# Kernel optimization log

Measured on AMD Instinct MI355X. Metric: run time of the kernel, lower is better.

Reference implementation:

```python
import jax, jax.numpy as jnp
import numpy as np

N_NODES = 50000
N_EDGES = 800000
N_GRAPHS = 64
EPS = 1e-5
NEG_SLOPE = 0.2


def gat_conv(x, src, dst, W, a_src, a_dst, bias, heads, ch):
    # x: [N, Fin]; W: [Fin, heads*ch]; a_src/a_dst: [heads, ch]; bias: [heads*ch]
    N = x.shape[0]
    h = (x @ W).reshape(N, heads, ch)                       # [N,H,C]
    s_src = jnp.sum(h * a_src, axis=-1)                     # [N,H]
    s_dst = jnp.sum(h * a_dst, axis=-1)                     # [N,H]
    scores = jax.nn.leaky_relu(s_src[src] + s_dst[dst], NEG_SLOPE)  # [E,H]
    m = jax.ops.segment_max(scores, dst, num_segments=N)    # segment softmax (stable)
    e = jnp.exp(scores - m[dst])
    denom = jax.ops.segment_sum(e, dst, num_segments=N)
    alpha = e / denom[dst]                                  # [E,H]
    msg = h[src] * alpha[:, :, None]                        # [E,H,C]
    out = jax.ops.segment_sum(msg, dst, num_segments=N)     # [N,H,C]
    return out.reshape(N, heads * ch) + bias


def batch_norm(x, gamma, beta):
    mu = jnp.mean(x, axis=0)
    var = jnp.var(x, axis=0)  # biased, as in torch BN forward (training mode)
    return gamma * (x - mu) * jax.lax.rsqrt(var + EPS) + beta


def setup_inputs() -> dict:
    key = jax.random.key(0)
    ks = jax.random.split(key, 20)
    x = jax.random.normal(ks[0], (N_NODES, 8), dtype=jnp.float32)
    edge_index = jax.random.randint(ks[1], (2, N_EDGES), 0, N_NODES, dtype=jnp.int32)
    batch = jnp.sort(jax.random.randint(ks[2], (N_NODES,), 0, N_GRAPHS, dtype=jnp.int32))
    g = lambda k, shape: jax.random.normal(k, shape, dtype=jnp.float32) * 0.1
    return {
        "x": x, "edge_index": edge_index, "batch": batch,
        "W1": g(ks[3], (8, 128)), "a_src1": g(ks[4], (4, 32)), "a_dst1": g(ks[5], (4, 32)),
        "b1": jnp.zeros((128,), jnp.float32), "g1": jnp.ones((128,), jnp.float32),
        "beta1": jnp.zeros((128,), jnp.float32),
        "W2": g(ks[6], (128, 256)), "a_src2": g(ks[7], (4, 64)), "a_dst2": g(ks[8], (4, 64)),
        "b2": jnp.zeros((256,), jnp.float32), "g2": jnp.ones((256,), jnp.float32),
        "beta2": jnp.zeros((256,), jnp.float32),
        "fc1_w": g(ks[9], (256, 128)), "fc1_b": jnp.zeros((128,), jnp.float32),
        "fc2_w": g(ks[10], (128, 64)), "fc2_b": jnp.zeros((64,), jnp.float32),
        "fc3_w": g(ks[11], (64, 1)), "fc3_b": jnp.zeros((1,), jnp.float32),
    }


def reference(x, edge_index, batch, W1, a_src1, a_dst1, b1, g1, beta1,
              W2, a_src2, a_dst2, b2, g2, beta2,
              fc1_w, fc1_b, fc2_w, fc2_b, fc3_w, fc3_b):
    N = x.shape[0]
    loop = jnp.arange(N, dtype=edge_index.dtype)
    src = jnp.concatenate([edge_index[0], loop])  # PyG GATConv adds self-loops
    dst = jnp.concatenate([edge_index[1], loop])

    h = gat_conv(x, src, dst, W1, a_src1, a_dst1, b1, heads=4, ch=32)
    h = jax.nn.elu(batch_norm(h, g1, beta1))
    h = gat_conv(h, src, dst, W2, a_src2, a_dst2, b2, heads=4, ch=64)
    h = jax.nn.elu(batch_norm(h, g2, beta2))

    # global mean pool over graphs
    sums = jax.ops.segment_sum(h, batch, num_segments=N_GRAPHS)
    counts = jax.ops.segment_sum(jnp.ones((N,), h.dtype), batch, num_segments=N_GRAPHS)
    pooled = sums / jnp.maximum(counts, 1.0)[:, None]       # [G,256]

    z = jax.nn.relu(pooled @ fc1_w + fc1_b)
    emb = jax.nn.relu(z @ fc2_w + fc2_b)
    out = emb @ fc3_w + fc3_b
    return out.reshape(-1)
```

## Files before the change

kernel.cpp:

```cpp
#include <hip/hip_runtime.h>
#include <hip/hip_bf16.h>
#include <cmath>

#define NSLOPE 0.2f
#define BN_EPS 1e-5f
#define DEGCAP 128

static __device__ __forceinline__ float lrelu(float v) { return v > 0.f ? v : NSLOPE * v; }

static __device__ __forceinline__ float wmax64(float v) {
#pragma unroll
  for (int off = 32; off; off >>= 1) v = fmaxf(v, __shfl_xor(v, off));
  return v;
}
static __device__ __forceinline__ float wsum64(float v) {
#pragma unroll
  for (int off = 32; off; off >>= 1) v += __shfl_xor(v, off);
  return v;
}
static __device__ __forceinline__ unsigned short f2bf(float x) {
  __hip_bfloat16 h = __float2bfloat16(x);
  union { __hip_bfloat16 h; unsigned short u; } c; c.h = h; return c.u;
}
static __device__ __forceinline__ unsigned pack_bf16(float x, float y) {
  return (unsigned)f2bf(x) | ((unsigned)f2bf(y) << 16);
}
static __device__ __forceinline__ float bflo(unsigned p) { return __uint_as_float(p << 16); }
static __device__ __forceinline__ float bfhi(unsigned p) { return __uint_as_float(p & 0xffff0000u); }

__global__ void k_scatter(const int* __restrict__ esrc, const int* __restrict__ edst,
                          const int* __restrict__ batch, int E, int N,
                          int* __restrict__ cnt, int* __restrict__ srcs,
                          int* __restrict__ gstart,
                          const float* __restrict__ W1, const float* __restrict__ as1,
                          const float* __restrict__ ad1, const float* __restrict__ W2,
                          const float* __restrict__ as2, const float* __restrict__ ad2,
                          float* __restrict__ q1s, float* __restrict__ q1d,
                          float* __restrict__ q2s, float* __restrict__ q2d) {
  if (blockIdx.x == 0) {
    int t = threadIdx.x;
    if (t < 32) {
      int k = t >> 2, h = t & 3;
      float s = 0.f, d = 0.f;
      for (int c = 0; c < 32; ++c) {
        float w = W1[k * 128 + h * 32 + c];
        s = fmaf(w, as1[h * 32 + c], s);
        d = fmaf(w, ad1[h * 32 + c], d);
      }
      q1s[t] = s; q1d[t] = d;
    }
    for (int idx = t; idx < 512; idx += 256) {
      int k = idx >> 2, h = idx & 3;
      float s = 0.f, d = 0.f;
      for (int c = 0; c < 64; ++c) {
        float w = W2[k * 256 + h * 64 + c];
        s = fmaf(w, as2[h * 64 + c], s);
        d = fmaf(w, ad2[h * 64 + c], d);
      }
      q2s[idx] = s; q2d[idx] = d;
    }
  }
  int i = blockIdx.x * blockDim.x + threadIdx.x;
  int stride = gridDim.x * blockDim.x;
  int total = E + N;
  for (int j = i; j < total; j += stride) {
    int s, d;
    if (j < E) {
      s = esrc[j]; d = edst[j];
    } else {
      int n = j - E;
      s = n; d = n;
      int b = batch[n];
      if (n == 0) {
        for (int g = 0; g <= b; ++g) gstart[g] = 0;
      } else {
        int pb = batch[n - 1];
        if (pb != b)
          for (int g = pb + 1; g <= b; ++g) gstart[g] = n;
      }
      if (n == N - 1)
        for (int g = b + 1; g <= 64; ++g) gstart[g] = N;
    }
    int pos = atomicAdd(&cnt[d], 1);
    if (pos < DEGCAP) srcs[(size_t)d * DEGCAP + pos] = s;
  }
}

__global__ __launch_bounds__(256) void k_s1(const float* __restrict__ x,
                                            const float* __restrict__ q1s,
                                            const float* __restrict__ q1d,
                                            float* __restrict__ ssrc, float* __restrict__ sdst,
                                            int N) {
  __shared__ float qs[32], qd[32];
  int t = threadIdx.x;
  if (t < 32) { qs[t] = q1s[t]; qd[t] = q1d[t]; }
  __syncthreads();
  for (int n = blockIdx.x * 256 + t; n < N; n += gridDim.x * 256) {
    float4 x0 = *(const float4*)&x[n * 8];
    float4 x1 = *(const float4*)&x[n * 8 + 4];
    float xs[8] = {x0.x, x0.y, x0.z, x0.w, x1.x, x1.y, x1.z, x1.w};
    float4 rs = make_float4(0.f, 0.f, 0.f, 0.f);
    float4 rd = make_float4(0.f, 0.f, 0.f, 0.f);
#pragma unroll
    for (int k = 0; k < 8; ++k) {
      rs.x = fmaf(xs[k], qs[k * 4 + 0], rs.x);
      rs.y = fmaf(xs[k], qs[k * 4 + 1], rs.y);
      rs.z = fmaf(xs[k], qs[k * 4 + 2], rs.z);
      rs.w = fmaf(xs[k], qs[k * 4 + 3], rs.w);
      rd.x = fmaf(xs[k], qd[k * 4 + 0], rd.x);
      rd.y = fmaf(xs[k], qd[k * 4 + 1], rd.y);
      rd.z = fmaf(xs[k], qd[k * 4 + 2], rd.z);
      rd.w = fmaf(xs[k], qd[k * 4 + 3], rd.w);
    }
    *(float4*)&ssrc[n * 4] = rs;
    *(float4*)&sdst[n * 4] = rd;
  }
}

__global__ __launch_bounds__(256) void k_agg1(const float* __restrict__ x,
                                              const float* __restrict__ ssrc,
                                              const float* __restrict__ sdst,
                                              const int* __restrict__ cnt,
                                              const int* __restrict__ srcs,
                                              float* __restrict__ agg , int N) {
  int tid = blockIdx.x * 256 + threadIdx.x;
  int n = tid >> 2, h = tid & 3;
  if (n >= N) return;
  int beg = n * DEGCAP;
  int end = beg + min(cnt[n], DEGCAP);
  float sd = sdst[n * 4 + h];
  float m = -INFINITY;
  for (int e = beg; e < end; ++e) {
    int s = srcs[e];
    m = fmaxf(m, lrelu(ssrc[s * 4 + h] + sd));
  }
  float d = 0.f;
  float acc[8];
#pragma unroll
  for (int k = 0; k < 8; ++k) acc[k] = 0.f;
  const float4* x4 = (const float4*)x;
  for (int e = beg; e < end; ++e) {
    int s = srcs[e];
    float w = expf(lrelu(ssrc[s * 4 + h] + sd) - m);
    d += w;
    float4 xa = x4[(size_t)s * 2];
    float4 xb = x4[(size_t)s * 2 + 1];
    acc[0] = fmaf(w, xa.x, acc[0]); acc[1] = fmaf(w, xa.y, acc[1]);
    acc[2] = fmaf(w, xa.z, acc[2]); acc[3] = fmaf(w, xa.w, acc[3]);
    acc[4] = fmaf(w, xb.x, acc[4]); acc[5] = fmaf(w, xb.y, acc[5]);
    acc[6] = fmaf(w, xb.z, acc[6]); acc[7] = fmaf(w, xb.w, acc[7]);
  }
  float inv = 1.0f / d;
  float4 oA = make_float4(acc[0] * inv, acc[1] * inv, acc[2] * inv, acc[3] * inv);
  float4 oB = make_float4(acc[4] * inv, acc[5] * inv, acc[6] * inv, acc[7] * inv);
  *(float4*)&agg[n * 32 + h * 8] = oA;
  *(float4*)&agg[n * 32 + h * 8 + 4] = oB;
}

__global__ __launch_bounds__(128) void k_stats1(const float* __restrict__ agg,
                                                const float* __restrict__ W1,
                                                const float* __restrict__ b1,
                                                float* __restrict__ part, int N) {
  int t = threadIdx.x;
  __shared__ float ag[32];
  float bb = b1[t];
  float wc[8];
#pragma unroll
  for (int k = 0; k < 8; ++k) wc[k] = W1[k * 128 + t];
  int h = t >> 5;
  float s = 0.f, s2 = 0.f;
  for (int n = blockIdx.x; n < N; n += gridDim.x) {
    if (t < 32) ag[t] = agg[n * 32 + t];
    __syncthreads();
    float v = bb;
#pragma unroll
    for (int k = 0; k < 8; ++k) v = fmaf(ag[h * 8 + k], wc[k], v);
    s += v; s2 += v * v;
    __syncthreads();
  }
  part[(size_t)blockIdx.x * 256 + t] = s;
  part[(size_t)blockIdx.x * 256 + 128 + t] = s2;
}

template <int NB, int TWO_F>
__global__ __launch_bounds__(256) void k_bnreduce2(const float* __restrict__ part,
                                                   float* __restrict__ stat) {
  int j = blockIdx.x, t = threadIdx.x;
  float s = 0.f;
  for (int b = t; b < NB; b += 256) s += part[(size_t)b * TWO_F + j];
#pragma unroll
  for (int off = 32; off; off >>= 1) s += __shfl_xor(s, off);
  __shared__ float red[4];
  if ((t & 63) == 0) red[t >> 6] = s;
  __syncthreads();
  if (t == 0) stat[j] = (red[0] + red[1]) + (red[2] + red[3]);
}

__global__ __launch_bounds__(256) void k_bns2(const float* __restrict__ agg,
                                              const float* __restrict__ W1,
                                              const float* __restrict__ b1,
                                              unsigned* __restrict__ a1h_u,
                                              const float* __restrict__ sum,
                                              const float* __restrict__ sq,
                                              const float* __restrict__ gamma,
                                              const float* __restrict__ beta,
                                              const float* __restrict__ q2s,
                                              const float* __restrict__ q2d,
                                              float* __restrict__ ssrc2,
                                              float* __restrict__ sdst2, int N) {
  int w = threadIdx.x >> 6, l = threadIdx.x & 63;
  int n = blockIdx.x * 4 + w;
  if (n >= N) return;
  int c0 = 2 * l, c1 = 2 * l + 1;
  int h = l >> 4;
  float ag[8];
#pragma unroll
  for (int k = 0; k < 8; ++k) ag[k] = agg[n * 32 + h * 8 + k];
  float v0 = b1[c0], v1 = b1[c1];
#pragma unroll
  for (int k = 0; k < 8; ++k) {
    v0 = fmaf(ag[k], W1[k * 128 + c0], v0);
    v1 = fmaf(ag[k], W1[k * 128 + c1], v1);
  }
  float invN = 1.0f / N;
  float mean0 = sum[c0] * invN, mean1 = sum[c1] * invN;
  float var0 = sq[c0] * invN - mean0 * mean0;
  float var1 = sq[c1] * invN - mean1 * mean1;
  float iv0 = rsqrtf(var0 + BN_EPS), iv1 = rsqrtf(var1 + BN_EPS);
  float y0 = gamma[c0] * ((v0 - mean0) * iv0) + beta[c0];
  float y1 = gamma[c1] * ((v1 - mean1) * iv1) + beta[c1];
  y0 = y0 > 0.f ? y0 : expm1f(y0);
  y1 = y1 > 0.f ? y1 : expm1f(y1);
  a1h_u[(size_t)n * 64 + l] = pack_bf16(y0, y1);
  float4 qs0 = *(const float4*)&q2s[c0 * 4];
  float4 qs1 = *(const float4*)&q2s[c1 * 4];
  float4 qd0 = *(const float4*)&q2d[c0 * 4];
  float4 qd1 = *(const float4*)&q2d[c1 * 4];
  float p0 = fmaf(y1, qs1.x, y0 * qs0.x);
  float p1 = fmaf(y1, qs1.y, y0 * qs0.y);
  float p2 = fmaf(y1, qs1.z, y0 * qs0.z);
  float p3 = fmaf(y1, qs1.w, y0 * qs0.w);
  float d0 = fmaf(y1, qd1.x, y0 * qd0.x);
  float d1 = fmaf(y1, qd1.y, y0 * qd0.y);
  float d2 = fmaf(y1, qd1.z, y0 * qd0.z);
  float d3 = fmaf(y1, qd1.w, y0 * qd0.w);
#pragma unroll
  for (int off = 32; off; off >>= 1) {
    p0 += __shfl_xor(p0, off); p1 += __shfl_xor(p1, off);
    p2 += __shfl_xor(p2, off); p3 += __shfl_xor(p3, off);
    d0 += __shfl_xor(d0, off); d1 += __shfl_xor(d1, off);
    d2 += __shfl_xor(d2, off); d3 += __shfl_xor(d3, off);
  }
  if (l == 0) {
    *(float4*)&ssrc2[n * 4] = make_float4(p0, p1, p2, p3);
    *(float4*)&sdst2[n * 4] = make_float4(d0, d1, d2, d3);
  }
}

__global__ __launch_bounds__(256) void k_agg2(const unsigned* __restrict__ a1h_u,
                                              const float* __restrict__ ssrc,
                                              const float* __restrict__ sdst,
                                              const int* __restrict__ cnt,
                                              const int* __restrict__ srcs,
                                              unsigned* __restrict__ aggh , int N) {
  __shared__ float evl[4][64][4];
  __shared__ int sil[4][64];
  int wid = threadIdx.x >> 6, l = threadIdx.x & 63;
  int n = blockIdx.x * 4 + wid;
  if (n >= N) return;
  int beg = n * DEGCAP;
  int deg = min(cnt[n], DEGCAP);
  float4 sd = *(const float4*)&sdst[n * 4];
  float m0 = -INFINITY, m1 = -INFINITY, m2 = -INFINITY, m3 = -INFINITY;
  float d0 = 0.f, d1 = 0.f, d2 = 0.f, d3 = 0.f;
  float2 ac0 = {0.f, 0.f}, ac1 = {0.f, 0.f}, ac2 = {0.f, 0.f}, ac3 = {0.f, 0.f};
  for (int c0 = 0; c0 < deg; c0 += 64) {
    int e = c0 + l;
    bool act = e < deg;
    int s = act ? srcs[beg + e] : 0;
    float4 sv = *(const float4*)&ssrc[s * 4];
    float v0 = act ? lrelu(sv.x + sd.x) : -INFINITY;
    float v1 = act ? lrelu(sv.y + sd.y) : -INFINITY;
    float v2 = act ? lrelu(sv.z + sd.z) : -INFINITY;
    float v3 = act ? lrelu(sv.w + sd.w) : -INFINITY;
    float nm0 = fmaxf(m0, wmax64(v0)), nm1 = fmaxf(m1, wmax64(v1));
    float nm2 = fmaxf(m2, wmax64(v2)), nm3 = fmaxf(m3, wmax64(v3));
    float sc0 = expf(m0 - nm0), sc1 = expf(m1 - nm1);
    float sc2 = expf(m2 - nm2), sc3 = expf(m3 - nm3);
    m0 = nm0; m1 = nm1; m2 = nm2; m3 = nm3;
    float ev0 = act ? expf(v0 - m0) : 0.f;
    float ev1 = act ? expf(v1 - m1) : 0.f;
    float ev2 = act ? expf(v2 - m2) : 0.f;
    float ev3 = act ? expf(v3 - m3) : 0.f;
    d0 = d0 * sc0 + wsum64(ev0);
    d1 = d1 * sc1 + wsum64(ev1);
    d2 = d2 * sc2 + wsum64(ev2);
    d3 = d3 * sc3 + wsum64(ev3);
    ac0.x *= sc0; ac0.y *= sc0; ac1.x *= sc1; ac1.y *= sc1;
    ac2.x *= sc2; ac2.y *= sc2; ac3.x *= sc3; ac3.y *= sc3;
    *(float4*)&evl[wid][l][0] = make_float4(ev0, ev1, ev2, ev3);
    sil[wid][l] = s;
    int cn = min(64, deg - c0);
    int cn4 = (cn + 3) & ~3;
    for (int j = 0; j < cn4; j += 4) {
      int4 s4 = *(const int4*)&sil[wid][j];
      float4 wA = *(const float4*)&evl[wid][j][0];
      float4 wB = *(const float4*)&evl[wid][j + 1][0];
      float4 wC = *(const float4*)&evl[wid][j + 2][0];
      float4 wD = *(const float4*)&evl[wid][j + 3][0];
      unsigned pA = a1h_u[(size_t)s4.x * 64 + l];
      unsigned pB = a1h_u[(size_t)s4.y * 64 + l];
      unsigned pC = a1h_u[(size_t)s4.z * 64 + l];
      unsigned pD = a1h_u[(size_t)s4.w * 64 + l];
      float ax, ay;
      ax = bflo(pA); ay = bfhi(pA);
      ac0.x = fmaf(wA.x, ax, ac0.x); ac0.y = fmaf(wA.x, ay, ac0.y);
      ac1.x = fmaf(wA.y, ax, ac1.x); ac1.y = fmaf(wA.y, ay, ac1.y);
      ac2.x = fmaf(wA.z, ax, ac2.x); ac2.y = fmaf(wA.z, ay, ac2.y);
      ac3.x = fmaf(wA.w, ax, ac3.x); ac3.y = fmaf(wA.w, ay, ac3.y);
      ax = bflo(pB); ay = bfhi(pB);
      ac0.x = fmaf(wB.x, ax, ac0.x); ac0.y = fmaf(wB.x, ay, ac0.y);
      ac1.x = fmaf(wB.y, ax, ac1.x); ac1.y = fmaf(wB.y, ay, ac1.y);
      ac2.x = fmaf(wB.z, ax, ac2.x); ac2.y = fmaf(wB.z, ay, ac2.y);
      ac3.x = fmaf(wB.w, ax, ac3.x); ac3.y = fmaf(wB.w, ay, ac3.y);
      ax = bflo(pC); ay = bfhi(pC);
      ac0.x = fmaf(wC.x, ax, ac0.x); ac0.y = fmaf(wC.x, ay, ac0.y);
      ac1.x = fmaf(wC.y, ax, ac1.x); ac1.y = fmaf(wC.y, ay, ac1.y);
      ac2.x = fmaf(wC.z, ax, ac2.x); ac2.y = fmaf(wC.z, ay, ac2.y);
      ac3.x = fmaf(wC.w, ax, ac3.x); ac3.y = fmaf(wC.w, ay, ac3.y);
      ax = bflo(pD); ay = bfhi(pD);
      ac0.x = fmaf(wD.x, ax, ac0.x); ac0.y = fmaf(wD.x, ay, ac0.y);
      ac1.x = fmaf(wD.y, ax, ac1.x); ac1.y = fmaf(wD.y, ay, ac1.y);
      ac2.x = fmaf(wD.z, ax, ac2.x); ac2.y = fmaf(wD.z, ay, ac2.y);
      ac3.x = fmaf(wD.w, ax, ac3.x); ac3.y = fmaf(wD.w, ay, ac3.y);
    }
  }
  size_t pl = (size_t)N * 64;
  size_t base = (size_t)n * 64 + l;
  float i0 = 1.0f / d0, i1 = 1.0f / d1, i2 = 1.0f / d2, i3 = 1.0f / d3;
  aggh[base] = pack_bf16(ac0.x * i0, ac0.y * i0);
  aggh[pl + base] = pack_bf16(ac1.x * i1, ac1.y * i1);
  aggh[2 * pl + base] = pack_bf16(ac2.x * i2, ac2.y * i2);
  aggh[3 * pl + base] = pack_bf16(ac3.x * i3, ac3.y * i3);
}

__global__ __launch_bounds__(256) void k_post2(const unsigned short* __restrict__ aggh,
                                               const float* __restrict__ W2,
                                               const float* __restrict__ b2,
                                               unsigned* __restrict__ o2h,
                                               float* __restrict__ part, int N) {
  __shared__ float As[64][64];
  __shared__ float Bs[64][64];
  int h = blockIdx.y;
  int m0 = blockIdx.x * 64;
  int tid = threadIdx.x;
  const unsigned short* Ap = aggh + (size_t)h * N * 128;
  int tx = tid & 15, ty = tid >> 4;
  float acc[4][4];
#pragma unroll
  for (int r = 0; r < 4; ++r)
#pragma unroll
    for (int c = 0; c < 4; ++c) acc[r][c] = 0.f;

#pragma unroll
  for (int kc = 0; kc < 2; ++kc) {
    {
      int ml = tid & 63, kg = tid >> 6;
      const unsigned short* arow = Ap + (size_t)(m0 + ml) * 128 + kc * 64 + kg * 16;
      bool rok = (m0 + ml) < N;
#pragma unroll
      for (int it = 0; it < 2; ++it) {
        uint4 q = rok ? *(const uint4*)(arow + it * 8) : make_uint4(0, 0, 0, 0);
        int kb = kg * 16 + it * 8;
        As[kb + 0][ml] = bflo(q.x); As[kb + 1][ml] = bfhi(q.x);
        As[kb + 2][ml] = bflo(q.y); As[kb + 3][ml] = bfhi(q.y);
        As[kb + 4][ml] = bflo(q.z); As[kb + 5][ml] = bfhi(q.z);
        As[kb + 6][ml] = bflo(q.w); As[kb + 7][ml] = bfhi(q.w);
      }
    }
    {
      int c4 = tid & 15, k0 = tid >> 4;
      for (int k = k0; k < 64; k += 16) {
        float4 v = *(const float4*)&W2[(size_t)(kc * 64 + k) * 256 + h * 64 + c4 * 4];
        *(float4*)&Bs[k][c4 * 4] = v;
      }
    }
    __syncthreads();
#pragma unroll 2
    for (int k = 0; k < 64; ++k) {
      float4 a4 = *(const float4*)&As[k][ty * 4];
      float4 b4 = *(const float4*)&Bs[k][tx * 4];
      float av[4] = {a4.x, a4.y, a4.z, a4.w};
      float bv[4] = {b4.x, b4.y, b4.z, b4.w};
#pragma unroll
      for (int r = 0; r < 4; ++r)
#pragma unroll
        for (int c = 0; c < 4; ++c) acc[r][c] = fmaf(av[r], bv[c], acc[r][c]);
    }
    __syncthreads();
  }

  float4 bb = *(const float4*)&b2[h * 64 + tx * 4];
  float ps[4] = {0.f, 0.f, 0.f, 0.f};
  float pq[4] = {0.f, 0.f, 0.f, 0.f};
#pragma unroll
  for (int r = 0; r < 4; ++r) {
    int row = m0 + ty * 4 + r;
    if (row < N) {
      float4 c4;
      c4.x = acc[r][0] + bb.x; c4.y = acc[r][1] + bb.y;
      c4.z = acc[r][2] + bb.z; c4.w = acc[r][3] + bb.w;
      uint2 pw;
      pw.x = pack_bf16(c4.x, c4.y);
      pw.y = pack_bf16(c4.z, c4.w);
      *(uint2*)&o2h[(size_t)row * 128 + (h * 64 + tx * 4) / 2] = pw;
      ps[0] += c4.x; pq[0] += c4.x * c4.x;
      ps[1] += c4.y; pq[1] += c4.y * c4.y;
      ps[2] += c4.z; pq[2] += c4.z * c4.z;
      ps[3] += c4.w; pq[3] += c4.w * c4.w;
    }
  }
  __syncthreads();
  float* red = &As[0][0];
#pragma unroll
  for (int c = 0; c < 4; ++c) {
    red[ty * 64 + tx * 4 + c] = ps[c];
    red[1024 + ty * 64 + tx * 4 + c] = pq[c];
  }
  __syncthreads();
  if (tid < 128) {
    int isq = tid >> 6, col = tid & 63;
    float s = 0.f;
#pragma unroll
    for (int w = 0; w < 16; ++w) s += red[isq * 1024 + w * 64 + col];
    part[((size_t)blockIdx.x * 4 + h) * 128 + isq * 64 + col] = s;
  }
}

__global__ __launch_bounds__(256) void k_bnredpost(const float* __restrict__ part, int nmb,
                                                   float* __restrict__ stat) {
  int j = blockIdx.x;
  int isq = j >> 8, col = j & 255;
  int h = col >> 6, cw = col & 63;
  int t = threadIdx.x;
  float s = 0.f;
  for (int mb = t; mb < nmb; mb += 256) s += part[((size_t)mb * 4 + h) * 128 + isq * 64 + cw];
#pragma unroll
  for (int off = 32; off; off >>= 1) s += __shfl_xor(s, off);
  __shared__ float red[4];
  if ((t & 63) == 0) red[t >> 6] = s;
  __syncthreads();
  if (t == 0) stat[j] = (red[0] + red[1]) + (red[2] + red[3]);
}

__global__ __launch_bounds__(256) void k_poolbn(const unsigned* __restrict__ o2h,
                                                const int* __restrict__ gstart,
                                                const float* __restrict__ sum,
                                                const float* __restrict__ sq,
                                                const float* __restrict__ gamma,
                                                const float* __restrict__ beta,
                                                float* __restrict__ part, int N) {
  int g = blockIdx.x, by = blockIdx.y, t = threadIdx.x;
  float mean = sum[t] * (1.0f / N);
  float var = sq[t] * (1.0f / N) - mean * mean;
  float inv = rsqrtf(var + BN_EPS);
  float ga = gamma[t], be = beta[t];
  int r0 = gstart[g], r1 = gstart[g + 1];
  int u = t >> 1, hi = t & 1;
  float s = 0.f;
  for (int base = r0 + by * 128; base < r1; base += 16 * 128) {
    int lim = min(r1, base + 128);
    for (int r = base; r < lim; ++r) {
      unsigned pw = o2h[(size_t)r * 128 + u];
      float v = hi ? bfhi(pw) : bflo(pw);
      float y = ga * ((v - mean) * inv) + be;
      s += (y > 0.f ? y : expm1f(y));
    }
  }
  part[((size_t)g * 16 + by) * 256 + t] = s;
}

__global__ __launch_bounds__(256) void k_head(const float* __restrict__ poolpart,
                                              const int* __restrict__ gstart,
                                              const float* __restrict__ w1, const float* __restrict__ b1,
                                              const float* __restrict__ w2, const float* __restrict__ b2,
                                              const float* __restrict__ w3, const float* __restrict__ b3,
                                              float* __restrict__ out) {
  __shared__ float p[256], z1[128], z2[64];
  int g = blockIdx.x, t = threadIdx.x;
  float s0 = 0.f;
#pragma unroll
  for (int b = 0; b < 16; ++b) s0 += poolpart[((size_t)g * 16 + b) * 256 + t];
  float cnt = (float)(gstart[g + 1] - gstart[g]);
  p[t] = s0 / fmaxf(cnt, 1.0f);
  __syncthreads();
  if (t < 128) {
    float s = b1[t];
    for (int k = 0; k < 256; ++k) s = fmaf(p[k], w1[k * 128 + t], s);
    z1[t] = fmaxf(s, 0.f);
  }
  __syncthreads();
  if (t < 64) {
    float s = b2[t];
    for (int k = 0; k < 128; ++k) s = fmaf(z1[k], w2[k * 64 + t], s);
    z2[t] = fmaxf(s, 0.f);
  }
  __syncthreads();
  if (t < 64) {
    float s = z2[t] * w3[t];
#pragma unroll
    for (int off = 32; off; off >>= 1) s += __shfl_xor(s, off);
    if (t == 0) out[g] = s + b3[0];
  }
}

extern "C" void kernel_launch(void* const* d_in, const int* in_sizes, int n_in,
                              void* d_out, int out_size, void* d_ws, size_t ws_size,
                              hipStream_t stream) {
  const float* x    = (const float*)d_in[0];
  const int*   eidx = (const int*)d_in[1];
  const int*   batch= (const int*)d_in[2];
  const float* W1   = (const float*)d_in[3];
  const float* as1  = (const float*)d_in[4];
  const float* ad1  = (const float*)d_in[5];
  const float* b1   = (const float*)d_in[6];
  const float* g1   = (const float*)d_in[7];
  const float* be1  = (const float*)d_in[8];
  const float* W2   = (const float*)d_in[9];
  const float* as2  = (const float*)d_in[10];
  const float* ad2  = (const float*)d_in[11];
  const float* b2   = (const float*)d_in[12];
  const float* g2   = (const float*)d_in[13];
  const float* be2  = (const float*)d_in[14];
  const float* fc1w = (const float*)d_in[15];
  const float* fc1b = (const float*)d_in[16];
  const float* fc2w = (const float*)d_in[17];
  const float* fc2b = (const float*)d_in[18];
  const float* fc3w = (const float*)d_in[19];
  const float* fc3b = (const float*)d_in[20];
  float* out = (float*)d_out;
  (void)n_in; (void)out_size; (void)ws_size;

  int N = in_sizes[0] / 8;
  int E = in_sizes[1] / 2;
  const int* esrc = eidx;
  const int* edst = eidx + E;
  int nmb = (N + 63) / 64;

  char* w = (char*)d_ws;
  auto take = [&](size_t bytes) -> char* {
    char* r = w;
    w += (bytes + 255) & ~(size_t)255;
    return r;
  };
  int*   cnt     = (int*)take(4 * (size_t)N);
  int*   srcs    = (int*)take(4 * (size_t)N * DEGCAP);
  int*   gstart  = (int*)take(4 * 65);
  float* bnstat  = (float*)take(4 * 1024);
  float* bnpart  = (float*)take(4 * 524288);
  float* pp2     = (float*)take(4 * (size_t)nmb * 512);
  float* poolpart= (float*)take(4 * 64 * 16 * 256);
  float* q1s     = (float*)take(4 * 32);
  float* q1d     = (float*)take(4 * 32);
  float* q2s     = (float*)take(4 * 512);
  float* q2d     = (float*)take(4 * 512);
  float* ssrc1   = (float*)take(16 * (size_t)N);
  float* sdst1   = (float*)take(16 * (size_t)N);
  float* ssrc2   = (float*)take(16 * (size_t)N);
  float* sdst2   = (float*)take(16 * (size_t)N);
  float* agg1    = (float*)take(4 * (size_t)N * 32);
  unsigned short* a1h  = (unsigned short*)take(2 * (size_t)N * 128);
  unsigned short* aggh = (unsigned short*)take(2 * (size_t)N * 512);
  unsigned* o2h  = (unsigned*)take(4 * (size_t)N * 128);

  float* sum1 = bnstat;       float* sq1 = bnstat + 128;
  float* sum2 = bnstat + 256; float* sq2 = bnstat + 512;

  hipMemsetAsync(cnt, 0, 4 * (size_t)N, stream);
  k_scatter<<<2048, 256, 0, stream>>>(esrc, edst, batch, E, N, cnt, srcs, gstart,
                                      W1, as1, ad1, W2, as2, ad2, q1s, q1d, q2s, q2d);

  k_s1<<<256, 256, 0, stream>>>(x, q1s, q1d, ssrc1, sdst1, N);
  k_agg1<<<(4 * N + 255) / 256, 256, 0, stream>>>(x, ssrc1, sdst1, cnt, srcs, agg1, N);
  k_stats1<<<2048, 128, 0, stream>>>(agg1, W1, b1, bnpart, N);
  k_bnreduce2<2048, 256><<<256, 256, 0, stream>>>(bnpart, bnstat);
  k_bns2<<<(N + 3) / 4, 256, 0, stream>>>(agg1, W1, b1, (unsigned*)a1h, sum1, sq1, g1, be1,
                                          q2s, q2d, ssrc2, sdst2, N);

  k_agg2<<<(N + 3) / 4, 256, 0, stream>>>((const unsigned*)a1h, ssrc2, sdst2, cnt, srcs,
                                          (unsigned*)aggh, N);
  k_post2<<<dim3(nmb, 4), 256, 0, stream>>>(aggh, W2, b2, o2h, pp2, N);
  k_bnredpost<<<512, 256, 0, stream>>>(pp2, nmb, sum2);

  k_poolbn<<<dim3(64, 16), 256, 0, stream>>>(o2h, gstart, sum2, sq2, g2, be2, poolpart, N);
  k_head<<<64, 256, 0, stream>>>(poolpart, gstart, fc1w, fc1b, fc2w, fc2b, fc3w, fc3b, out);
}
```

Measured before the change: 326.1 us.

## Replace LDS staging in layer-2 aggregation with readlane broadcasts and packed FMA

Rewrites the layer-2 GAT aggregation kernel to handle up to 128 edges (the DEGCAP limit) in two fixed 64-lane halves. The max and denominator are computed once, which removes the online-softmax rescaling. Edge indices and weights are broadcast with readlane into scalar registers instead of going through shared memory, and the accumulators use 2-wide vector FMA so the compiler can emit packed FP32 instructions. This removes LDS traffic and the rescale multiplies, but adds many readlane ops and raises register pressure.

```diff
diff --git a/kernel.cpp b/kernel.cpp
--- a/kernel.cpp
+++ b/kernel.cpp
@@ -6,6 +6,8 @@
 #define BN_EPS 1e-5f
 #define DEGCAP 128
 
+typedef float v2f __attribute__((ext_vector_type(2)));
+
 static __device__ __forceinline__ float lrelu(float v) { return v > 0.f ? v : NSLOPE * v; }
 
 static __device__ __forceinline__ float wmax64(float v) {
@@ -17,6 +19,9 @@
 #pragma unroll
   for (int off = 32; off; off >>= 1) v += __shfl_xor(v, off);
   return v;
+}
+static __device__ __forceinline__ float rlf(float v, int j) {
+  return __int_as_float(__builtin_amdgcn_readlane(__float_as_int(v), j));
 }
 static __device__ __forceinline__ unsigned short f2bf(float x) {
   __hip_bfloat16 h = __float2bfloat16(x);
@@ -263,76 +268,119 @@
                                               const int* __restrict__ cnt,
                                               const int* __restrict__ srcs,
                                               unsigned* __restrict__ aggh , int N) {
-  __shared__ float evl[4][64][4];
-  __shared__ int sil[4][64];
   int wid = threadIdx.x >> 6, l = threadIdx.x & 63;
   int n = blockIdx.x * 4 + wid;
   if (n >= N) return;
   int beg = n * DEGCAP;
   int deg = min(cnt[n], DEGCAP);
   float4 sd = *(const float4*)&sdst[n * 4];
-  float m0 = -INFINITY, m1 = -INFINITY, m2 = -INFINITY, m3 = -INFINITY;
-  float d0 = 0.f, d1 = 0.f, d2 = 0.f, d3 = 0.f;
-  float2 ac0 = {0.f, 0.f}, ac1 = {0.f, 0.f}, ac2 = {0.f, 0.f}, ac3 = {0.f, 0.f};
-  for (int c0 = 0; c0 < deg; c0 += 64) {
-    int e = c0 + l;
-    bool act = e < deg;
-    int s = act ? srcs[beg + e] : 0;
-    float4 sv = *(const float4*)&ssrc[s * 4];
-    float v0 = act ? lrelu(sv.x + sd.x) : -INFINITY;
-    float v1 = act ? lrelu(sv.y + sd.y) : -INFINITY;
-    float v2 = act ? lrelu(sv.z + sd.z) : -INFINITY;
-    float v3 = act ? lrelu(sv.w + sd.w) : -INFINITY;
-    float nm0 = fmaxf(m0, wmax64(v0)), nm1 = fmaxf(m1, wmax64(v1));
-    float nm2 = fmaxf(m2, wmax64(v2)), nm3 = fmaxf(m3, wmax64(v3));
-    float sc0 = expf(m0 - nm0), sc1 = expf(m1 - nm1);
-    float sc2 = expf(m2 - nm2), sc3 = expf(m3 - nm3);
-    m0 = nm0; m1 = nm1; m2 = nm2; m3 = nm3;
-    float ev0 = act ? expf(v0 - m0) : 0.f;
-    float ev1 = act ? expf(v1 - m1) : 0.f;
-    float ev2 = act ? expf(v2 - m2) : 0.f;
-    float ev3 = act ? expf(v3 - m3) : 0.f;
-    d0 = d0 * sc0 + wsum64(ev0);
-    d1 = d1 * sc1 + wsum64(ev1);
-    d2 = d2 * sc2 + wsum64(ev2);
-    d3 = d3 * sc3 + wsum64(ev3);
-    ac0.x *= sc0; ac0.y *= sc0; ac1.x *= sc1; ac1.y *= sc1;
-    ac2.x *= sc2; ac2.y *= sc2; ac3.x *= sc3; ac3.y *= sc3;
-    *(float4*)&evl[wid][l][0] = make_float4(ev0, ev1, ev2, ev3);
-    sil[wid][l] = s;
-    int cn = min(64, deg - c0);
+  bool actA = l < deg;
+  bool actB = 64 + l < deg;
+  int sA_ = actA ? srcs[beg + l] : 0;
+  int sB_ = actB ? srcs[beg + 64 + l] : 0;
+  float4 svA = *(const float4*)&ssrc[sA_ * 4];
+  float4 svB = *(const float4*)&ssrc[sB_ * 4];
+  float vA0 = actA ? lrelu(svA.x + sd.x) : -INFINITY;
+  float vA1 = actA ? lrelu(svA.y + sd.y) : -INFINITY;
+  float vA2 = actA ? lrelu(svA.z + sd.z) : -INFINITY;
+  float vA3 = actA ? lrelu(svA.w + sd.w) : -INFINITY;
+  float vB0 = actB ? lrelu(svB.x + sd.x) : -INFINITY;
+  float vB1 = actB ? lrelu(svB.y + sd.y) : -INFINITY;
+  float vB2 = actB ? lrelu(svB.z + sd.z) : -INFINITY;
+  float vB3 = actB ? lrelu(svB.w + sd.w) : -INFINITY;
+  float m0 = wmax64(fmaxf(vA0, vB0));
+  float m1 = wmax64(fmaxf(vA1, vB1));
+  float m2 = wmax64(fmaxf(vA2, vB2));
+  float m3 = wmax64(fmaxf(vA3, vB3));
+  float eA0 = actA ? expf(vA0 - m0) : 0.f;
+  float eA1 = actA ? expf(vA1 - m1) : 0.f;
+  float eA2 = actA ? expf(vA2 - m2) : 0.f;
+  float eA3 = actA ? expf(vA3 - m3) : 0.f;
+  float eB0 = actB ? expf(vB0 - m0) : 0.f;
+  float eB1 = actB ? expf(vB1 - m1) : 0.f;
+  float eB2 = actB ? expf(vB2 - m2) : 0.f;
+  float eB3 = actB ? expf(vB3 - m3) : 0.f;
+  float d0 = wsum64(eA0 + eB0);
+  float d1 = wsum64(eA1 + eB1);
+  float d2 = wsum64(eA2 + eB2);
+  float d3 = wsum64(eA3 + eB3);
+  v2f ac0 = {0.f, 0.f}, ac1 = {0.f, 0.f}, ac2 = {0.f, 0.f}, ac3 = {0.f, 0.f};
+  {
+    int cn = min(deg, 64);
     int cn4 = (cn + 3) & ~3;
     for (int j = 0; j < cn4; j += 4) {
-      int4 s4 = *(const int4*)&sil[wid][j];
-      float4 wA = *(const float4*)&evl[wid][j][0];
-      float4 wB = *(const float4*)&evl[wid][j + 1][0];
-      float4 wC = *(const float4*)&evl[wid][j + 2][0];
-      float4 wD = *(const float4*)&evl[wid][j + 3][0];
-      unsigned pA = a1h_u[(size_t)s4.x * 64 + l];
-      unsigned pB = a1h_u[(size_t)s4.y * 64 + l];
-      unsigned pC = a1h_u[(size_t)s4.z * 64 + l];
-      unsigned pD = a1h_u[(size_t)s4.w * 64 + l];
-      float ax, ay;
-      ax = bflo(pA); ay = bfhi(pA);
-      ac0.x = fmaf(wA.x, ax, ac0.x); ac0.y = fmaf(wA.x, ay, ac0.y);
-      ac1.x = fmaf(wA.y, ax, ac1.x); ac1.y = fmaf(wA.y, ay, ac1.y);
-      ac2.x = fmaf(wA.z, ax, ac2.x); ac2.y = fmaf(wA.z, ay, ac2.y);
-      ac3.x = fmaf(wA.w, ax, ac3.x); ac3.y = fmaf(wA.w, ay, ac3.y);
-      ax = bflo(pB); ay = bfhi(pB);
-      ac0.x = fmaf(wB.x, ax, ac0.x); ac0.y = fmaf(wB.x, ay, ac0.y);
-      ac1.x = fmaf(wB.y, ax, ac1.x); ac1.y = fmaf(wB.y, ay, ac1.y);
-      ac2.x = fmaf(wB.z, ax, ac2.x); ac2.y = fmaf(wB.z, ay, ac2.y);
-      ac3.x = fmaf(wB.w, ax, ac3.x); ac3.y = fmaf(wB.w, ay, ac3.y);
-      ax = bflo(pC); ay = bfhi(pC);
-      ac0.x = fmaf(wC.x, ax, ac0.x); ac0.y = fmaf(wC.x, ay, ac0.y);
-      ac1.x = fmaf(wC.y, ax, ac1.x); ac1.y = fmaf(wC.y, ay, ac1.y);
-      ac2.x = fmaf(wC.z, ax, ac2.x); ac2.y = fmaf(wC.z, ay, ac2.y);
-      ac3.x = fmaf(wC.w, ax, ac3.x); ac3.y = fmaf(wC.w, ay, ac3.y);
-      ax = bflo(pD); ay = bfhi(pD);
-      ac0.x = fmaf(wD.x, ax, ac0.x); ac0.y = fmaf(wD.x, ay, ac0.y);
-      ac1.x = fmaf(wD.y, ax, ac1.x); ac1.y = fmaf(wD.y, ay, ac1.y);
-      ac2.x = fmaf(wD.z, ax, ac2.x); ac2.y = fmaf(wD.z, ay, ac2.y);
-      ac3.x = fmaf(wD.w, ax, ac3.x); ac3.y = fmaf(wD.w, ay, ac3.y);
+      int iA = __builtin_amdgcn_readlane(sA_, j);
+      int iB = __builtin_amdgcn_readlane(sA_, j + 1);
+      int iC = __builtin_amdgcn_readlane(sA_, j + 2);
+      int iD = __builtin_amdgcn_readlane(sA_, j + 3);
+      unsigned pA = a1h_u[(size_t)iA * 64 + l];
+      unsigned pB = a1h_u[(size_t)iB * 64 + l];
+      unsigned pC = a1h_u[(size_t)iC * 64 + l];
+      unsigned pD = a1h_u[(size_t)iD * 64 + l];
+      float wA0 = rlf(eA0, j),     wA1 = rlf(eA1, j),     wA2 = rlf(eA2, j),     wA3 = rlf(eA3, j);
+      float wB0 = rlf(eA0, j + 1), wB1 = rlf(eA1, j + 1), wB2 = rlf(eA2, j + 1), wB3 = rlf(eA3, j + 1);
+      float wC0 = rlf(eA0, j + 2), wC1 = rlf(eA1, j + 2), wC2 = rlf(eA2, j + 2), wC3 = rlf(eA3, j + 2);
+      float wD0 = rlf(eA0, j + 3), wD1 = rlf(eA1, j + 3), wD2 = rlf(eA2, j + 3), wD3 = rlf(eA3, j + 3);
+      v2f av;
+      av = (v2f){bflo(pA), bfhi(pA)};
+      ac0 = __builtin_elementwise_fma((v2f){wA0, wA0}, av, ac0);
+      ac1 = __builtin_elementwise_fma((v2f){wA1, wA1}, av, ac1);
+      ac2 = __builtin_elementwise_fma((v2f){wA2, wA2}, av, ac2);
+      ac3 = __builtin_elementwise_fma((v2f){wA3, wA3}, av, ac3);
+      av = (v2f){bflo(pB), bfhi(pB)};
+      ac0 = __builtin_elementwise_fma((v2f){wB0, wB0}, av, ac0);
+      ac1 = __builtin_elementwise_fma((v2f){wB1, wB1}, av, ac1);
+      ac2 = __builtin_elementwise_fma((v2f){wB2, wB2}, av, ac2);
+      ac3 = __builtin_elementwise_fma((v2f){wB3, wB3}, av, ac3);
+      av = (v2f){bflo(pC), bfhi(pC)};
+      ac0 = __builtin_elementwise_fma((v2f){wC0, wC0}, av, ac0);
+      ac1 = __builtin_elementwise_fma((v2f){wC1, wC1}, av, ac1);
+      ac2 = __builtin_elementwise_fma((v2f){wC2, wC2}, av, ac2);
+      ac3 = __builtin_elementwise_fma((v2f){wC3, wC3}, av, ac3);
+      av = (v2f){bflo(pD), bfhi(pD)};
+      ac0 = __builtin_elementwise_fma((v2f){wD0, wD0}, av, ac0);
+      ac1 = __builtin_elementwise_fma((v2f){wD1, wD1}, av, ac1);
+      ac2 = __builtin_elementwise_fma((v2f){wD2, wD2}, av, ac2);
+      ac3 = __builtin_elementwise_fma((v2f){wD3, wD3}, av, ac3);
+    }
+  }
+  if (deg > 64) {
+    int cn = deg - 64;
+    int cn4 = (cn + 3) & ~3;
+    for (int j = 0; j < cn4; j += 4) {
+      int iA = __builtin_amdgcn_readlane(sB_, j);
+      int iB = __builtin_amdgcn_readlane(sB_, j + 1);
+      int iC = __builtin_amdgcn_readlane(sB_, j + 2);
+      int iD = __builtin_amdgcn_readlane(sB_, j + 3);
+      unsigned pA = a1h_u[(size_t)iA * 64 + l];
+      unsigned pB = a1h_u[(size_t)iB * 64 + l];
+      unsigned pC = a1h_u[(size_t)iC * 64 + l];
+      unsigned pD = a1h_u[(size_t)iD * 64 + l];
+      float wA0 = rlf(eB0, j),     wA1 = rlf(eB1, j),     wA2 = rlf(eB2, j),     wA3 = rlf(eB3, j);
+      float wB0 = rlf(eB0, j + 1), wB1 = rlf(eB1, j + 1), wB2 = rlf(eB2, j + 1), wB3 = rlf(eB3, j + 1);
+      float wC0 = rlf(eB0, j + 2), wC1 = rlf(eB1, j + 2), wC2 = rlf(eB2, j + 2), wC3 = rlf(eB3, j + 2);
+      float wD0 = rlf(eB0, j + 3), wD1 = rlf(eB1, j + 3), wD2 = rlf(eB2, j + 3), wD3 = rlf(eB3, j + 3);
+      v2f av;
+      av = (v2f){bflo(pA), bfhi(pA)};
+      ac0 = __builtin_elementwise_fma((v2f){wA0, wA0}, av, ac0);
+      ac1 = __builtin_elementwise_fma((v2f){wA1, wA1}, av, ac1);
+      ac2 = __builtin_elementwise_fma((v2f){wA2, wA2}, av, ac2);
+      ac3 = __builtin_elementwise_fma((v2f){wA3, wA3}, av, ac3);
+      av = (v2f){bflo(pB), bfhi(pB)};
+      ac0 = __builtin_elementwise_fma((v2f){wB0, wB0}, av, ac0);
+      ac1 = __builtin_elementwise_fma((v2f){wB1, wB1}, av, ac1);
+      ac2 = __builtin_elementwise_fma((v2f){wB2, wB2}, av, ac2);
+      ac3 = __builtin_elementwise_fma((v2f){wB3, wB3}, av, ac3);
+      av = (v2f){bflo(pC), bfhi(pC)};
+      ac0 = __builtin_elementwise_fma((v2f){wC0, wC0}, av, ac0);
+      ac1 = __builtin_elementwise_fma((v2f){wC1, wC1}, av, ac1);
+      ac2 = __builtin_elementwise_fma((v2f){wC2, wC2}, av, ac2);
+      ac3 = __builtin_elementwise_fma((v2f){wC3, wC3}, av, ac3);
+      av = (v2f){bflo(pD), bfhi(pD)};
+      ac0 = __builtin_elementwise_fma((v2f){wD0, wD0}, av, ac0);
+      ac1 = __builtin_elementwise_fma((v2f){wD1, wD1}, av, ac1);
+      ac2 = __builtin_elementwise_fma((v2f){wD2, wD2}, av, ac2);
+      ac3 = __builtin_elementwise_fma((v2f){wD3, wD3}, av, ac3);
     }
   }
   size_t pl = (size_t)N * 64;
```

Measured after the change: 316.4 us. 1.03x faster.
